# Optimization experiments

Measured on AMD Instinct MI355X. Metric: run time of the kernel, lower is better.

Reference implementation:

```python
import jax, jax.numpy as jnp
import numpy as np

B, T, D_MODEL, HEAD_SIZE = 8, 1024, 1024, 64
BLOCK_SIZE = 1024  # == max_relative_pos


def setup_inputs() -> dict:
    key = jax.random.key(0)
    ks = jax.random.split(key, 7)
    s = 1.0 / np.sqrt(D_MODEL)
    return {
        "x": jax.random.normal(ks[0], (B, T, D_MODEL), dtype=jnp.float32),
        "Wk": jax.random.normal(ks[1], (D_MODEL, HEAD_SIZE), dtype=jnp.float32) * s,
        "bk": jax.random.normal(ks[2], (HEAD_SIZE,), dtype=jnp.float32) * 0.02,
        "Wq": jax.random.normal(ks[3], (D_MODEL, HEAD_SIZE), dtype=jnp.float32) * s,
        "bq": jax.random.normal(ks[4], (HEAD_SIZE,), dtype=jnp.float32) * 0.02,
        "Wv": jax.random.normal(ks[5], (D_MODEL, HEAD_SIZE), dtype=jnp.float32) * s,
        "rel_emb": jax.random.normal(ks[6], (2 * BLOCK_SIZE + 1, HEAD_SIZE), dtype=jnp.float32) * 0.02,
        "mask": 1,
    }


def reference(x, Wk, bk, Wq, bq, Wv, rel_emb, mask):
    Bb, Tt, _ = x.shape
    hs = Wk.shape[1]
    max_rel = (rel_emb.shape[0] - 1) // 2

    k = x @ Wk + bk          # [B,T,hs]
    q = x @ Wq + bq          # [B,T,hs]
    v = x @ Wv               # [B,T,hs]

    pos = jnp.arange(Tt)
    idx = jnp.clip(pos[:, None] - pos[None, :], -max_rel, max_rel) + max_rel
    r = rel_emb[idx]         # [T,T,hs], r[i,j] = emb(clip(i-j))

    # scores[b,i,j] = (q[b,i] + r[i,j]) . (k[b,j] + r[j,i]) / sqrt(hs)
    scale = 1.0 / np.sqrt(hs).astype(np.float32)
    scores = (
        jnp.einsum("bid,bjd->bij", q, k)
        + jnp.einsum("bid,jid->bij", q, r)   # q_i . r[j,i]
        + jnp.einsum("ijd,bjd->bij", r, k)   # r[i,j] . k_j
        + jnp.einsum("ijd,jid->ij", r, r)[None]  # r[i,j] . r[j,i]
    ) * scale

    if mask:  # static Python int -> causal mask, matches tril masked_fill
        causal = jnp.tril(jnp.ones((Tt, Tt), dtype=bool))
        scores = jnp.where(causal, scores, jnp.float32(-jnp.inf))

    w = jax.nn.softmax(scores, axis=-1)  # dropout is identity in eval mode
    return w @ v  # [B,T,hs]
```

## Files before the change

### kernel.cpp

```cpp
#include <hip/hip_runtime.h>
#include <hip/hip_bf16.h>
#include <math.h>


typedef __hip_bfloat16 bf16;
typedef __attribute__((ext_vector_type(8))) short short8;
typedef __attribute__((ext_vector_type(4))) float f32x4;

#define NTRI 136
#define MFMA16(a, b, c) __builtin_amdgcn_mfma_f32_16x16x32_bf16(a, b, c, 0, 0, 0)

__device__ __forceinline__ float bf2f(bf16 h) { return __bfloat162float(h); }
__device__ __forceinline__ bf16 f2bf(float f) { return __float2bfloat16(f); }
__device__ __forceinline__ short bfs(float f) {
  bf16 h = __float2bfloat16(f);
  return *(short*)&h;
}

union U16 {
  uint4 u;
  short8 s;
};
__device__ __forceinline__ short8 ldfrag(const bf16* p) {
  U16 x;
  x.u = *(const uint4*)p;
  return x.s;
}

__global__ void wt_kernel(const float* __restrict__ Wk, const float* __restrict__ Wq,
                          const float* __restrict__ Wv, bf16* __restrict__ WT) {
  int idx = blockIdx.x * 256 + threadIdx.x;
  int sel = idx >> 16, r = idx & 65535;
  int n = r >> 10, kk = r & 1023;
  const float* W = (sel == 0) ? Wk : (sel == 1) ? Wq : Wv;
  WT[idx] = f2bf(W[kk * 64 + n]);
}

__global__ void ecast_kernel(const float* __restrict__ E, bf16* __restrict__ Ep,
                             bf16* __restrict__ Erev) {
  int idx = blockIdx.x * 256 + threadIdx.x;
  if (idx >= 2049 * 64) return;
  int t = idx >> 6, d = idx & 63;
  Ep[idx] = f2bf(E[idx]);
  Erev[idx] = f2bf(E[(2048 - t) * 64 + d]);
}

__global__ void rr_kernel(const float* __restrict__ E, float* __restrict__ rrG) {
  int dlt = blockIdx.x;
  int d = threadIdx.x;
  float p = E[(size_t)(1024 + dlt) * 64 + d] * E[(size_t)(1024 - dlt) * 64 + d];
#pragma unroll
  for (int off = 32; off > 0; off >>= 1) p += __shfl_down(p, off);
  if (d == 0) rrG[64 + dlt] = p;
}

__global__ __launch_bounds__(128) void qkv_mfma(
    const float* __restrict__ x, const bf16* __restrict__ WT,
    const float* __restrict__ bk, const float* __restrict__ bq,
    bf16* __restrict__ qB, bf16* __restrict__ kB, bf16* __restrict__ vT) {
  const int R0 = blockIdx.x << 5;
  const int t = threadIdx.x;
  const int lane = t & 63, wave = t >> 6;
  const int m = lane & 15, quad = lane >> 4;
  const int strip = wave << 4;

  __shared__ bf16 VTS[64][40];

  const float* xrow = x + (size_t)(R0 + strip + m) * 1024;
  f32x4 acc[3][4];
#pragma unroll
  for (int s = 0; s < 3; ++s)
#pragma unroll
    for (int c = 0; c < 4; ++c) acc[s][c] = (f32x4){0.f, 0.f, 0.f, 0.f};

  for (int ks = 0; ks < 32; ++ks) {
    const int k0 = ks * 32 + quad * 8;
    float4 xa = *(const float4*)(xrow + k0);
    float4 xb = *(const float4*)(xrow + k0 + 4);
    short8 a;
    a[0] = bfs(xa.x); a[1] = bfs(xa.y); a[2] = bfs(xa.z); a[3] = bfs(xa.w);
    a[4] = bfs(xb.x); a[5] = bfs(xb.y); a[6] = bfs(xb.z); a[7] = bfs(xb.w);
#pragma unroll
    for (int sel = 0; sel < 3; ++sel)
#pragma unroll
      for (int ct = 0; ct < 4; ++ct) {
        const bf16* bb = WT + ((size_t)(sel * 64 + ct * 16 + m) << 10) + ks * 32 + quad * 8;
        acc[sel][ct] = MFMA16(a, ldfrag(bb), acc[sel][ct]);
      }
  }

#pragma unroll
  for (int ct = 0; ct < 4; ++ct) {
    const int col = ct * 16 + m;
    const float bkv = bk[col], bqv = bq[col];
#pragma unroll
    for (int r = 0; r < 4; ++r) {
      const int lrow = strip + quad * 4 + r;
      const size_t grow = (size_t)(R0 + lrow);
      kB[grow * 64 + col] = f2bf(acc[0][ct][r] + bkv);
      qB[grow * 64 + col] = f2bf(acc[1][ct][r] + bqv);
      VTS[col][lrow] = f2bf(acc[2][ct][r]);
    }
  }
  __syncthreads();
  {
    const int dd = t >> 1, h = (t & 1) << 4;
    const int b = R0 >> 10, tloc = R0 & 1023;
    uint4* dst = (uint4*)(vT + ((size_t)(b * 64 + dd) << 10) + tloc + h);
    dst[0] = *(const uint4*)&VTS[dd][h + 0];
    dst[1] = *(const uint4*)&VTS[dd][h + 8];
  }
}

__global__ __launch_bounds__(256, 3) void flash_mfma(
    const bf16* __restrict__ qB, const bf16* __restrict__ kB, const bf16* __restrict__ vT,
    const bf16* __restrict__ Ep, const bf16* __restrict__ Erev, const float* __restrict__ rrG,
    float* __restrict__ ml, float* __restrict__ Opart) {
  const int bx = blockIdx.x;
  const int b = bx / NTRI;
  const int rr_ = bx - b * NTRI;
  int it = (int)((sqrtf(8.f * rr_ + 1.f) - 1.f) * 0.5f);
  while ((it + 1) * (it + 2) / 2 <= rr_) ++it;
  while (it * (it + 1) / 2 > rr_) --it;
  const int jt = rr_ - it * (it + 1) / 2;
  const int I0 = it << 6, J0 = jt << 6;
  const int D = I0 - J0, w0 = D - 64;
  const int slot = bx;

  const int t = threadIdx.x;
  const int lane = t & 63, wave = t >> 6;
  const int m = lane & 15, quad = lane >> 4;
  const int strip = wave << 4;

  __shared__ bf16 M2S[64][136];
  __shared__ bf16 M3S[64][136];
  __shared__ __align__(16) bf16 PS[64][80];
  __shared__ float rrS[128];

  if (t < 128) rrS[t] = rrG[64 + w0 + t];

  const bf16* qbase = qB + ((size_t)((b << 10) + I0 + strip + m) << 6);
  const short8 aq0 = ldfrag(qbase + quad * 8);
  const short8 aq1 = ldfrag(qbase + 32 + quad * 8);
  const bf16* kbase = kB + ((size_t)((b << 10) + J0 + strip + m) << 6);
  const short8 ak0 = ldfrag(kbase + quad * 8);
  const short8 ak1 = ldfrag(kbase + 32 + quad * 8);

  const bf16* erb = Erev + ((size_t)(1024 + w0) << 6);
#pragma unroll
  for (int ct = 0; ct < 8; ++ct) {
    const bf16* bb = erb + ((size_t)(ct * 16 + m) << 6) + quad * 8;
    f32x4 c = (f32x4){0.f, 0.f, 0.f, 0.f};
    c = MFMA16(aq0, ldfrag(bb), c);
    c = MFMA16(aq1, ldfrag(bb + 32), c);
#pragma unroll
    for (int r = 0; r < 4; ++r) M2S[strip + quad * 4 + r][ct * 16 + m] = f2bf(c[r]);
  }
  const bf16* epb = Ep + ((size_t)(1024 + w0) << 6);
#pragma unroll
  for (int ct = 0; ct < 8; ++ct) {
    const bf16* bb = epb + ((size_t)(ct * 16 + m) << 6) + quad * 8;
    f32x4 c = (f32x4){0.f, 0.f, 0.f, 0.f};
    c = MFMA16(ak0, ldfrag(bb), c);
    c = MFMA16(ak1, ldfrag(bb + 32), c);
#pragma unroll
    for (int r = 0; r < 4; ++r) M3S[strip + quad * 4 + r][ct * 16 + m] = f2bf(c[r]);
  }
  f32x4 acc[4];
#pragma unroll
  for (int ct = 0; ct < 4; ++ct) {
    const bf16* bb = kB + ((size_t)((b << 10) + J0 + ct * 16 + m) << 6) + quad * 8;
    f32x4 c = (f32x4){0.f, 0.f, 0.f, 0.f};
    c = MFMA16(aq0, ldfrag(bb), c);
    c = MFMA16(aq1, ldfrag(bb + 32), c);
    acc[ct] = c;
  }
  __syncthreads();

  float sc[4][4], mrow[4], lrow[4];
#pragma unroll
  for (int r = 0; r < 4; ++r) mrow[r] = -INFINITY;
#pragma unroll
  for (int ct = 0; ct < 4; ++ct) {
    const int uj = ct * 16 + m;
#pragma unroll
    for (int r = 0; r < 4; ++r) {
      const int ui = strip + quad * 4 + r;
      float s;
      if (ui - uj + D >= 0) {
        const int wi = ui - uj + 64;
        s = (acc[ct][r] + bf2f(M2S[ui][wi]) + bf2f(M3S[uj][wi]) + rrS[wi]) * 0.125f;
      } else {
        s = -INFINITY;
      }
      sc[ct][r] = s;
      mrow[r] = fmaxf(mrow[r], s);
    }
  }
#pragma unroll
  for (int r = 0; r < 4; ++r) {
#pragma unroll
    for (int off = 1; off < 16; off <<= 1) mrow[r] = fmaxf(mrow[r], __shfl_xor(mrow[r], off));
    lrow[r] = 0.f;
  }
#pragma unroll
  for (int ct = 0; ct < 4; ++ct)
#pragma unroll
    for (int r = 0; r < 4; ++r) {
      float p = __expf(sc[ct][r] - mrow[r]);
      sc[ct][r] = p;
      lrow[r] += p;
    }
#pragma unroll
  for (int r = 0; r < 4; ++r) {
#pragma unroll
    for (int off = 1; off < 16; off <<= 1) lrow[r] += __shfl_xor(lrow[r], off);
  }
  if (m == 0) {
#pragma unroll
    for (int r = 0; r < 4; ++r) {
      const int ui = strip + quad * 4 + r;
      ml[(size_t)slot * 128 + ui] = mrow[r];
      ml[(size_t)slot * 128 + 64 + ui] = lrow[r];
    }
  }
#pragma unroll
  for (int ct = 0; ct < 4; ++ct)
#pragma unroll
    for (int r = 0; r < 4; ++r) PS[strip + quad * 4 + r][ct * 16 + m] = f2bf(sc[ct][r]);
  __syncthreads();

  const short8 ap0 = ldfrag(&PS[strip + m][quad * 8]);
  const short8 ap1 = ldfrag(&PS[strip + m][32 + quad * 8]);
  float* ob = Opart + (size_t)slot * 4096;
#pragma unroll
  for (int ct = 0; ct < 4; ++ct) {
    const bf16* bb = vT + ((size_t)(b * 64 + ct * 16 + m) << 10) + J0 + quad * 8;
    f32x4 o = (f32x4){0.f, 0.f, 0.f, 0.f};
    o = MFMA16(ap0, ldfrag(bb), o);
    o = MFMA16(ap1, ldfrag(bb + 32), o);
#pragma unroll
    for (int r = 0; r < 4; ++r)
      ob[(size_t)(strip + quad * 4 + r) * 64 + ct * 16 + m] = o[r];
  }
}

__global__ __launch_bounds__(256) void combine_kernel(
    const float* __restrict__ ml, const float* __restrict__ Opart, float* __restrict__ out) {
  const int row = (blockIdx.x << 2) + (threadIdx.x >> 6);
  const int d = threadIdx.x & 63;
  const int b = row >> 10, i = row & 1023;
  const int it = i >> 6, ii = i & 63;
  const int base = b * NTRI + it * (it + 1) / 2;

  float mstar = -INFINITY;
  for (int jtt = 0; jtt <= it; ++jtt)
    mstar = fmaxf(mstar, ml[(size_t)(base + jtt) * 128 + ii]);
  float L = 0.f, O = 0.f;
  for (int jtt = 0; jtt <= it; ++jtt) {
    size_t slot = base + jtt;
    float w = __expf(ml[slot * 128 + ii] - mstar);
    L += w * ml[slot * 128 + 64 + ii];
    O += w * Opart[slot * 4096 + (size_t)ii * 64 + d];
  }
  out[(size_t)row * 64 + d] = O / L;
}

extern "C" void kernel_launch(void* const* d_in, const int* in_sizes, int n_in,
                              void* d_out, int out_size, void* d_ws, size_t ws_size,
                              hipStream_t stream) {
  const float* x = (const float*)d_in[0];
  const float* Wk = (const float*)d_in[1];
  const float* bk = (const float*)d_in[2];
  const float* Wq = (const float*)d_in[3];
  const float* bq = (const float*)d_in[4];
  const float* Wv = (const float*)d_in[5];
  const float* E = (const float*)d_in[6];
  float* out = (float*)d_out;

  float* wsf = (float*)d_ws;
  float* ml = wsf;
  float* Opart = wsf + 139264;
  float* rrG = wsf + 139264 + 4456448;
  bf16* qB = (bf16*)(rrG + 1152);
  bf16* kB = qB + 524288;
  bf16* vT = kB + 524288;
  bf16* Ep = vT + 524288;
  bf16* Erev = Ep + 131200;
  bf16* WT = Erev + 131200;

  wt_kernel<<<768, 256, 0, stream>>>(Wk, Wq, Wv, WT);
  ecast_kernel<<<513, 256, 0, stream>>>(E, Ep, Erev);
  rr_kernel<<<1024, 64, 0, stream>>>(E, rrG);
  qkv_mfma<<<256, 128, 0, stream>>>(x, WT, bk, bq, qB, kB, vT);
  flash_mfma<<<8 * NTRI, 256, 0, stream>>>(qB, kB, vT, Ep, Erev, rrG, ml, Opart);
  combine_kernel<<<2048, 256, 0, stream>>>(ml, Opart, out);
}
```

Before: 167.3 us.

## Fuse prep kernels, split-K QKV projection, fold rr into M2S, raise flash occupancy

```diff
diff --git a/kernel.cpp b/kernel.cpp
--- a/kernel.cpp
+++ b/kernel.cpp
@@ -27,92 +27,100 @@
   return x.s;
 }
 
-__global__ void wt_kernel(const float* __restrict__ Wk, const float* __restrict__ Wq,
-                          const float* __restrict__ Wv, bf16* __restrict__ WT) {
-  int idx = blockIdx.x * 256 + threadIdx.x;
-  int sel = idx >> 16, r = idx & 65535;
-  int n = r >> 10, kk = r & 1023;
-  const float* W = (sel == 0) ? Wk : (sel == 1) ? Wq : Wv;
-  WT[idx] = f2bf(W[kk * 64 + n]);
-}
-
-__global__ void ecast_kernel(const float* __restrict__ E, bf16* __restrict__ Ep,
-                             bf16* __restrict__ Erev) {
-  int idx = blockIdx.x * 256 + threadIdx.x;
-  if (idx >= 2049 * 64) return;
-  int t = idx >> 6, d = idx & 63;
-  Ep[idx] = f2bf(E[idx]);
-  Erev[idx] = f2bf(E[(2048 - t) * 64 + d]);
-}
-
-__global__ void rr_kernel(const float* __restrict__ E, float* __restrict__ rrG) {
-  int dlt = blockIdx.x;
-  int d = threadIdx.x;
-  float p = E[(size_t)(1024 + dlt) * 64 + d] * E[(size_t)(1024 - dlt) * 64 + d];
-#pragma unroll
-  for (int off = 32; off > 0; off >>= 1) p += __shfl_down(p, off);
-  if (d == 0) rrG[64 + dlt] = p;
-}
-
-__global__ __launch_bounds__(128) void qkv_mfma(
+__global__ __launch_bounds__(256) void prep_kernel(
+    const float* __restrict__ Wk, const float* __restrict__ Wq, const float* __restrict__ Wv,
+    const float* __restrict__ E, bf16* __restrict__ WT, bf16* __restrict__ Ep,
+    bf16* __restrict__ Erev, float* __restrict__ rrG) {
+  const int bid = blockIdx.x, t = threadIdx.x;
+  if (bid < 768) {
+    int idx = bid * 256 + t;
+    int sel = idx >> 16, r = idx & 65535;
+    int n = r >> 10, kk = r & 1023;
+    const float* W = (sel == 0) ? Wk : (sel == 1) ? Wq : Wv;
+    WT[idx] = f2bf(W[kk * 64 + n]);
+  } else if (bid < 1281) {
+    int idx = (bid - 768) * 256 + t;
+    if (idx < 2049 * 64) {
+      int tt = idx >> 6, d = idx & 63;
+      Ep[idx] = f2bf(E[idx]);
+      Erev[idx] = f2bf(E[(2048 - tt) * 64 + d]);
+    }
+  } else {
+    int dlt = ((bid - 1281) << 2) + (t >> 6);
+    int d = t & 63;
+    float p = E[(size_t)(1024 + dlt) * 64 + d] * E[(size_t)(1024 - dlt) * 64 + d];
+#pragma unroll
+    for (int off = 32; off > 0; off >>= 1) p += __shfl_down(p, off);
+    if (d == 0) rrG[64 + dlt] = p;
+  }
+}
+
+__global__ __launch_bounds__(256, 2) void qkv_mfma(
     const float* __restrict__ x, const bf16* __restrict__ WT,
     const float* __restrict__ bk, const float* __restrict__ bq,
     bf16* __restrict__ qB, bf16* __restrict__ kB, bf16* __restrict__ vT) {
-  const int R0 = blockIdx.x << 5;
+  const int R0 = blockIdx.x << 4;
   const int t = threadIdx.x;
   const int lane = t & 63, wave = t >> 6;
   const int m = lane & 15, quad = lane >> 4;
-  const int strip = wave << 4;
-
-  __shared__ bf16 VTS[64][40];
-
-  const float* xrow = x + (size_t)(R0 + strip + m) * 1024;
+
+  __shared__ float RED[4][16][196];
+  __shared__ bf16 VTS[64][24];
+
+  const float* xrow = x + (size_t)(R0 + m) * 1024 + (wave << 8);
   f32x4 acc[3][4];
 #pragma unroll
   for (int s = 0; s < 3; ++s)
 #pragma unroll
     for (int c = 0; c < 4; ++c) acc[s][c] = (f32x4){0.f, 0.f, 0.f, 0.f};
 
-  for (int ks = 0; ks < 32; ++ks) {
+#pragma unroll
+  for (int ks = 0; ks < 8; ++ks) {
     const int k0 = ks * 32 + quad * 8;
     float4 xa = *(const float4*)(xrow + k0);
     float4 xb = *(const float4*)(xrow + k0 + 4);
     short8 a;
     a[0] = bfs(xa.x); a[1] = bfs(xa.y); a[2] = bfs(xa.z); a[3] = bfs(xa.w);
     a[4] = bfs(xb.x); a[5] = bfs(xb.y); a[6] = bfs(xb.z); a[7] = bfs(xb.w);
+    const int kg = (wave << 8) + k0;
 #pragma unroll
     for (int sel = 0; sel < 3; ++sel)
 #pragma unroll
       for (int ct = 0; ct < 4; ++ct) {
-        const bf16* bb = WT + ((size_t)(sel * 64 + ct * 16 + m) << 10) + ks * 32 + quad * 8;
+        const bf16* bb = WT + ((size_t)(sel * 64 + ct * 16 + m) << 10) + kg;
         acc[sel][ct] = MFMA16(a, ldfrag(bb), acc[sel][ct]);
       }
   }
 
 #pragma unroll
-  for (int ct = 0; ct < 4; ++ct) {
-    const int col = ct * 16 + m;
-    const float bkv = bk[col], bqv = bq[col];
-#pragma unroll
-    for (int r = 0; r < 4; ++r) {
-      const int lrow = strip + quad * 4 + r;
-      const size_t grow = (size_t)(R0 + lrow);
-      kB[grow * 64 + col] = f2bf(acc[0][ct][r] + bkv);
-      qB[grow * 64 + col] = f2bf(acc[1][ct][r] + bqv);
-      VTS[col][lrow] = f2bf(acc[2][ct][r]);
-    }
+  for (int sel = 0; sel < 3; ++sel)
+#pragma unroll
+    for (int ct = 0; ct < 4; ++ct)
+#pragma unroll
+      for (int r = 0; r < 4; ++r)
+        RED[wave][quad * 4 + r][sel * 64 + ct * 16 + m] = acc[sel][ct][r];
+  __syncthreads();
+
+#pragma unroll
+  for (int e = 0; e < 12; ++e) {
+    int idx = e * 256 + t;
+    int row = idx / 192, c = idx - row * 192;
+    float s = RED[0][row][c] + RED[1][row][c] + RED[2][row][c] + RED[3][row][c];
+    int sel = c >> 6, col = c & 63;
+    size_t grow = (size_t)(R0 + row);
+    if (sel == 0) kB[grow * 64 + col] = f2bf(s + bk[col]);
+    else if (sel == 1) qB[grow * 64 + col] = f2bf(s + bq[col]);
+    else VTS[col][row] = f2bf(s);
   }
   __syncthreads();
   {
-    const int dd = t >> 1, h = (t & 1) << 4;
-    const int b = R0 >> 10, tloc = R0 & 1023;
-    uint4* dst = (uint4*)(vT + ((size_t)(b * 64 + dd) << 10) + tloc + h);
-    dst[0] = *(const uint4*)&VTS[dd][h + 0];
-    dst[1] = *(const uint4*)&VTS[dd][h + 8];
-  }
-}
-
-__global__ __launch_bounds__(256, 3) void flash_mfma(
+    int dd = t >> 2, h = (t & 3) << 2;
+    int b = R0 >> 10, tloc = R0 & 1023;
+    *(uint2*)(vT + ((size_t)((b << 6) + dd) << 10) + tloc + h) = *(const uint2*)&VTS[dd][h];
+  }
+}
+
+__global__ __launch_bounds__(256, 4) void flash_mfma(
     const bf16* __restrict__ qB, const bf16* __restrict__ kB, const bf16* __restrict__ vT,
     const bf16* __restrict__ Ep, const bf16* __restrict__ Erev, const float* __restrict__ rrG,
     float* __restrict__ ml, float* __restrict__ Opart) {
@@ -132,12 +140,9 @@
   const int m = lane & 15, quad = lane >> 4;
   const int strip = wave << 4;
 
-  __shared__ bf16 M2S[64][136];
+  __shared__ __align__(16) bf16 M2S[64][136];
   __shared__ bf16 M3S[64][136];
-  __shared__ __align__(16) bf16 PS[64][80];
-  __shared__ float rrS[128];
-
-  if (t < 128) rrS[t] = rrG[64 + w0 + t];
+  bf16 (*PS)[80] = (bf16(*)[80])M2S;
 
   const bf16* qbase = qB + ((size_t)((b << 10) + I0 + strip + m) << 6);
   const short8 aq0 = ldfrag(qbase + quad * 8);
@@ -150,11 +155,12 @@
 #pragma unroll
   for (int ct = 0; ct < 8; ++ct) {
     const bf16* bb = erb + ((size_t)(ct * 16 + m) << 6) + quad * 8;
+    const float rv = rrG[64 + w0 + ct * 16 + m];
     f32x4 c = (f32x4){0.f, 0.f, 0.f, 0.f};
     c = MFMA16(aq0, ldfrag(bb), c);
     c = MFMA16(aq1, ldfrag(bb + 32), c);
 #pragma unroll
-    for (int r = 0; r < 4; ++r) M2S[strip + quad * 4 + r][ct * 16 + m] = f2bf(c[r]);
+    for (int r = 0; r < 4; ++r) M2S[strip + quad * 4 + r][ct * 16 + m] = f2bf(c[r] + rv);
   }
   const bf16* epb = Ep + ((size_t)(1024 + w0) << 6);
 #pragma unroll
@@ -189,7 +195,7 @@
       float s;
       if (ui - uj + D >= 0) {
         const int wi = ui - uj + 64;
-        s = (acc[ct][r] + bf2f(M2S[ui][wi]) + bf2f(M3S[uj][wi]) + rrS[wi]) * 0.125f;
+        s = (acc[ct][r] + bf2f(M2S[ui][wi]) + bf2f(M3S[uj][wi])) * 0.125f;
       } else {
         s = -INFINITY;
       }
@@ -224,6 +230,7 @@
       ml[(size_t)slot * 128 + 64 + ui] = lrow[r];
     }
   }
+  __syncthreads();
 #pragma unroll
   for (int ct = 0; ct < 4; ++ct)
 #pragma unroll
@@ -289,10 +296,8 @@
   bf16* Erev = Ep + 131200;
   bf16* WT = Erev + 131200;
 
-  wt_kernel<<<768, 256, 0, stream>>>(Wk, Wq, Wv, WT);
-  ecast_kernel<<<513, 256, 0, stream>>>(E, Ep, Erev);
-  rr_kernel<<<1024, 64, 0, stream>>>(E, rrG);
-  qkv_mfma<<<256, 128, 0, stream>>>(x, WT, bk, bq, qB, kB, vT);
+  prep_kernel<<<1537, 256, 0, stream>>>(Wk, Wq, Wv, E, WT, Ep, Erev, rrG);
+  qkv_mfma<<<512, 256, 0, stream>>>(x, WT, bk, bq, qB, kB, vT);
   flash_mfma<<<8 * NTRI, 256, 0, stream>>>(qB, kB, vT, Ep, Erev, rrG, ml, Opart);
   combine_kernel<<<2048, 256, 0, stream>>>(ml, Opart, out);
 }
```

Measured after the change: 156.9 us. 6.3% less time.
